# Performance work log

Measured on AMD Instinct MI355X. Metric: run time of the kernel, lower is better.

## Reference

```python
import jax, jax.numpy as jnp
import numpy as np

MODES = 16

def setup_inputs() -> dict:
    key = jax.random.key(0)
    k1, k2 = jax.random.split(key)
    x = jax.random.normal(k1, (16, 32, 256, 256), dtype=jnp.float32)
    weights = jax.random.normal(k2, (32, 32, MODES, MODES, 2), dtype=jnp.float32) * 0.1
    return {"x": x, "weights": weights}

def reference(x, weights):
    # x: [B, Ci, H, W]; weights: [Ci, Co, m, m, 2]
    B, Ci, H, W = x.shape
    m = weights.shape[2]
    Co = weights.shape[1]
    x_ft = jnp.fft.rfft2(x, axes=(-2, -1))  # [B, Ci, H, W//2+1] complex
    w_c = jax.lax.complex(weights[..., 0], weights[..., 1])  # [Ci, Co, m, m]
    low = jnp.einsum('bixy,ioxy->boxy', x_ft[:, :, :m, :m], w_c)  # [B, Co, m, m]
    out_ft = jnp.zeros((B, Co, H, W // 2 + 1), dtype=x_ft.dtype)
    out_ft = out_ft.at[:, :, :m, :m].set(low)
    return jnp.fft.irfft2(out_ft, s=(H, W), axes=(-2, -1)).astype(x.dtype)
```

## Files before the change

### kernel.cpp

```cpp
#include <hip/hip_runtime.h>

typedef float v4 __attribute__((ext_vector_type(4)));
typedef float f32x4 __attribute__((ext_vector_type(4)));
typedef short bf16x8 __attribute__((ext_vector_type(8)));

#define TWO_PI_256 0.024543692606170259f


__device__ __forceinline__ unsigned short f2bf(float f) {
  const unsigned int u = __float_as_uint(f);
  return (unsigned short)((u + 0x7fffu + ((u >> 16) & 1u)) >> 16);
}
__device__ __forceinline__ float bf2f(unsigned short h) {
  return __uint_as_float(((unsigned int)h) << 16);
}

__global__ __launch_bounds__(256) void k0_trig(unsigned short* __restrict__ Th,
                                               unsigned short* __restrict__ Tl,
                                               unsigned short* __restrict__ Bh,
                                               unsigned short* __restrict__ Bl) {
  const int k = threadIdx.x;
  const int o = blockIdx.x;
  {
    const int kx = o >> 1, p = o & 1;
    float sv, cv;
    sincosf((float)((kx * k) & 255) * TWO_PI_256, &sv, &cv);
    const float val = p ? -sv : cv;
    const unsigned short hi = f2bf(val);
    Th[o * 256 + k] = hi;
    Tl[o * 256 + k] = f2bf(val - bf2f(hi));
  }
  {
    const int idx = o * 256 + k;
    const int nt = idx >> 9;
    const int lane = (idx >> 3) & 63;
    const int j = idx & 7;
    const int q = lane >> 4;
    const int n16 = lane & 15;
    const int kk = q * 8 + j;
    const int w = nt * 16 + n16;
    float val;
    if (kk == 0) {
      val = 1.f / 65536.f;
    } else if (kk == 16) {
      val = 0.f;
    } else {
      const int kx = kk & 15;
      float sv, cv;
      sincosf((float)((kx * w) & 255) * TWO_PI_256, &sv, &cv);
      val = (kk < 16 ? 2.f * cv : -2.f * sv) * (1.f / 65536.f);
    }
    const unsigned short hi = f2bf(val);
    Bh[idx] = hi;
    Bl[idx] = f2bf(val - bf2f(hi));
  }
}

typedef __attribute__((address_space(1))) const unsigned int gas_u32;
typedef __attribute__((address_space(3))) unsigned int las_u32;

__global__ __launch_bounds__(256) void k12_dft(const float* __restrict__ x,
                                               const unsigned short* __restrict__ Th,
                                               const unsigned short* __restrict__ Tl,
                                               float* __restrict__ X) {
  __shared__ __align__(16) float SXF[256 * 34];
  __shared__ __align__(16) unsigned short Ts[2][32 * 264];
  const int tid = threadIdx.x;
  const int lane = tid & 63;
  const int w = tid >> 6;
  const long bc = blockIdx.x;
  {
    const int o = tid >> 3, kb = (tid & 7) * 32;
#pragma unroll
    for (int f = 0; f < 2; ++f) {
      const unsigned short* src = (f ? Tl : Th) + o * 256 + kb;
      unsigned short* dst = &Ts[f][o * 264 + kb];
#pragma unroll
      for (int j = 0; j < 32; j += 8)
        *(bf16x8*)(dst + j) = *(const bf16x8*)(src + j);
    }
  }
  const int q = lane >> 4;
  const int n16 = lane & 15;
  const int ucol = (lane & 7) ^ (lane >> 3);
  f32x4 acc[4][2] = {};
  for (int kc = 0; kc < 256; kc += 32) {
    __syncthreads();
#pragma unroll
    for (int i = 0; i < 8; ++i) {
      const int r0 = w * 64 + i * 8;
      __builtin_amdgcn_global_load_lds(
          (gas_u32*)(x + (bc * 256 + r0 + (lane >> 3)) * 256 + kc + ucol * 4),
          (las_u32*)((unsigned int*)SXF + r0 * 32), 16, 0, 0);
    }
    __syncthreads();
    bf16x8 bh[2], bl[2];
#pragma unroll
    for (int nt = 0; nt < 2; ++nt) {
      const int o = nt * 16 + n16;
      bh[nt] = *(const bf16x8*)&Ts[0][o * 264 + kc + q * 8];
      bl[nt] = *(const bf16x8*)&Ts[1][o * 264 + kc + q * 8];
    }
#pragma unroll
    for (int mt = 0; mt < 4; ++mt) {
      const int m = w * 64 + mt * 16 + n16;
      const int s = n16 & 7;
      const v4 a0 = *(const v4*)&SXF[m * 32 + ((2 * q) ^ s) * 4];
      const v4 a1 = *(const v4*)&SXF[m * 32 + ((2 * q + 1) ^ s) * 4];
      const float af[8] = {a0[0], a0[1], a0[2], a0[3], a1[0], a1[1], a1[2], a1[3]};
      bf16x8 ah, al;
#pragma unroll
      for (int j = 0; j < 8; ++j) {
        const unsigned short h = f2bf(af[j]);
        ah[j] = (short)h;
        al[j] = (short)f2bf(af[j] - bf2f(h));
      }
#pragma unroll
      for (int nt = 0; nt < 2; ++nt) {
        acc[mt][nt] = __builtin_amdgcn_mfma_f32_16x16x32_bf16(ah, bh[nt], acc[mt][nt], 0, 0, 0);
        acc[mt][nt] = __builtin_amdgcn_mfma_f32_16x16x32_bf16(al, bh[nt], acc[mt][nt], 0, 0, 0);
        acc[mt][nt] = __builtin_amdgcn_mfma_f32_16x16x32_bf16(ah, bl[nt], acc[mt][nt], 0, 0, 0);
      }
    }
  }
  __syncthreads();
#pragma unroll
  for (int mt = 0; mt < 4; ++mt)
#pragma unroll
    for (int nt = 0; nt < 2; ++nt)
#pragma unroll
      for (int r = 0; r < 4; ++r)
        SXF[(w * 64 + mt * 16 + q * 4 + r) * 34 + nt * 16 + n16] = acc[mt][nt][r];
  __syncthreads();
  {
    const int kx = tid & 15;
    const int ky = tid >> 4;
    float sn, cs;
    sincosf((float)ky * TWO_PI_256, &sn, &cs);
    float wr = 1.f, wi = 0.f;
    float xr = 0.f, xi = 0.f;
#pragma unroll 8
    for (int h = 0; h < 256; ++h) {
      const float2 f = *(const float2*)&SXF[h * 34 + 2 * kx];
      xr += f.x * wr + f.y * wi;
      xi += f.y * wr - f.x * wi;
      const float nwr = wr * cs - wi * sn;
      const float nwi = wr * sn + wi * cs;
      wr = nwr;
      wi = nwi;
    }
    *(float2*)&X[(bc * 256 + tid) * 2] = make_float2(xr, xi);
  }
}

__global__ __launch_bounds__(512) void kB_mixinv(const float* __restrict__ X,
                                                 const float* __restrict__ Wt,
                                                 const unsigned short* __restrict__ Bh,
                                                 const unsigned short* __restrict__ Bl,
                                                 float* __restrict__ out) {
  __shared__ float2 tbl[256];
  __shared__ float2 Yp[2][256];
  __shared__ float Gs[256][36];
  const int tid = threadIdx.x;
  const int lane = tid & 63;
  const int wv = tid >> 6;
  const int co = blockIdx.x;
  const int b = blockIdx.y;
  const long bc = b * 32 + co;
  const int t2 = tid & 255;
  const int hf = tid >> 8;
  if (hf == 0) {
    float sv, cv;
    sincosf((float)t2 * TWO_PI_256, &sv, &cv);
    tbl[t2] = make_float2(cv, sv);
  }
  {
    float yr = 0.f, yi = 0.f;
    const float2* Xp = (const float2*)X + ((long)b * 8192 + t2);
    const float2* Wp = (const float2*)Wt + ((long)co * 256 + t2);
#pragma unroll 8
    for (int ci = hf * 16; ci < hf * 16 + 16; ++ci) {
      const float2 xv = Xp[ci * 256];
      const float2 wv2 = Wp[ci * 8192];
      yr += xv.x * wv2.x - xv.y * wv2.y;
      yi += xv.x * wv2.y + xv.y * wv2.x;
    }
    Yp[hf][t2] = make_float2(yr, yi);
  }
  __syncthreads();
  if (tid < 256) {
    const float2 a = Yp[0][tid], c = Yp[1][tid];
    Yp[0][tid] = make_float2(a.x + c.x, a.y + c.y);
  }
  __syncthreads();
  {
    const int h = tid >> 1;
    const int p = tid & 1;
    float gr[8] = {}, gi[8] = {};
#pragma unroll 4
    for (int ky = 0; ky < 16; ++ky) {
      const float2 wt = tbl[(ky * h) & 255];
#pragma unroll
      for (int i = 0; i < 8; ++i) {
        const float2 yv = Yp[0][ky * 16 + p * 8 + i];
        gr[i] += yv.x * wt.x - yv.y * wt.y;
        gi[i] += yv.x * wt.y + yv.y * wt.x;
      }
    }
#pragma unroll
    for (int i = 0; i < 8; ++i) {
      const int kx = p * 8 + i;
      Gs[h][kx] = gr[i];
      Gs[h][16 + kx] = gi[i];
    }
  }
  __syncthreads();
  const int q = lane >> 4;
  const int n16 = lane & 15;
  bf16x8 ah[2], al[2];
#pragma unroll
  for (int mt = 0; mt < 2; ++mt) {
    const float* ap = &Gs[wv * 32 + mt * 16 + n16][q * 8];
    const v4 a0 = *(const v4*)ap;
    const v4 a1 = *(const v4*)(ap + 4);
    const float af[8] = {a0[0], a0[1], a0[2], a0[3], a1[0], a1[1], a1[2], a1[3]};
#pragma unroll
    for (int j = 0; j < 8; ++j) {
      const unsigned short hh = f2bf(af[j]);
      ah[mt][j] = (short)hh;
      al[mt][j] = (short)f2bf(af[j] - bf2f(hh));
    }
  }
  float* __restrict__ ob = out + bc * 65536;
#pragma unroll
  for (int nt = 0; nt < 16; ++nt) {
    const bf16x8 bhf = *(const bf16x8*)&Bh[(nt * 64 + lane) * 8];
    const bf16x8 blf = *(const bf16x8*)&Bl[(nt * 64 + lane) * 8];
    f32x4 c0 = {}, c1 = {};
    c0 = __builtin_amdgcn_mfma_f32_16x16x32_bf16(ah[0], bhf, c0, 0, 0, 0);
    c0 = __builtin_amdgcn_mfma_f32_16x16x32_bf16(al[0], bhf, c0, 0, 0, 0);
    c0 = __builtin_amdgcn_mfma_f32_16x16x32_bf16(ah[0], blf, c0, 0, 0, 0);
    c1 = __builtin_amdgcn_mfma_f32_16x16x32_bf16(ah[1], bhf, c1, 0, 0, 0);
    c1 = __builtin_amdgcn_mfma_f32_16x16x32_bf16(al[1], bhf, c1, 0, 0, 0);
    c1 = __builtin_amdgcn_mfma_f32_16x16x32_bf16(ah[1], blf, c1, 0, 0, 0);
#pragma unroll
    for (int r = 0; r < 4; ++r) {
      ob[(wv * 32 + q * 4 + r) * 256 + nt * 16 + n16] = c0[r];
      ob[(wv * 32 + 16 + q * 4 + r) * 256 + nt * 16 + n16] = c1[r];
    }
  }
}

extern "C" void kernel_launch(void* const* d_in, const int* in_sizes, int n_in,
                              void* d_out, int out_size, void* d_ws, size_t ws_size,
                              hipStream_t stream) {
  const float* x = (const float*)d_in[0];
  const float* wt = (const float*)d_in[1];
  float* out = (float*)d_out;
  float* X = (float*)d_ws;
  unsigned short* Th = (unsigned short*)(X + 262144);
  unsigned short* Tl = Th + 8192;
  unsigned short* Bh = Tl + 8192;
  unsigned short* Bl = Bh + 8192;
  k0_trig<<<32, 256, 0, stream>>>(Th, Tl, Bh, Bl);
  k12_dft<<<512, 256, 0, stream>>>(x, Th, Tl, X);
  kB_mixinv<<<dim3(32, 16), 512, 0, stream>>>(X, wt, Bh, Bl, out);
}
```

Measured before the change: 265.9 us.

## Fuse twiddle-table generation into DFT kernel and double its threads per block

Removes the separate trig-table kernel. Each DFT block now computes its own bf16 hi/lo cosine/sine table straight into shared memory during the first k-chunk, and the first 32 blocks also write the inverse-basis table used by the later mixing kernel. The block size grows from 256 to 512 threads, so each wave handles half as many rows. This drops one launch and a global round-trip for the tables, at the cost of redundant sincos work in every block and idle threads in the final column-DFT stage.

```diff
diff --git a/kernel.cpp b/kernel.cpp
--- a/kernel.cpp
+++ b/kernel.cpp
@@ -15,83 +15,68 @@
   return __uint_as_float(((unsigned int)h) << 16);
 }
 
-__global__ __launch_bounds__(256) void k0_trig(unsigned short* __restrict__ Th,
-                                               unsigned short* __restrict__ Tl,
+typedef __attribute__((address_space(1))) const unsigned int gas_u32;
+typedef __attribute__((address_space(3))) unsigned int las_u32;
+
+__global__ __launch_bounds__(512) void k12_dft(const float* __restrict__ x,
+                                               float* __restrict__ X,
                                                unsigned short* __restrict__ Bh,
                                                unsigned short* __restrict__ Bl) {
-  const int k = threadIdx.x;
-  const int o = blockIdx.x;
-  {
-    const int kx = o >> 1, p = o & 1;
-    float sv, cv;
-    sincosf((float)((kx * k) & 255) * TWO_PI_256, &sv, &cv);
-    const float val = p ? -sv : cv;
-    const unsigned short hi = f2bf(val);
-    Th[o * 256 + k] = hi;
-    Tl[o * 256 + k] = f2bf(val - bf2f(hi));
-  }
-  {
-    const int idx = o * 256 + k;
-    const int nt = idx >> 9;
-    const int lane = (idx >> 3) & 63;
-    const int j = idx & 7;
-    const int q = lane >> 4;
-    const int n16 = lane & 15;
-    const int kk = q * 8 + j;
-    const int w = nt * 16 + n16;
-    float val;
-    if (kk == 0) {
-      val = 1.f / 65536.f;
-    } else if (kk == 16) {
-      val = 0.f;
-    } else {
-      const int kx = kk & 15;
-      float sv, cv;
-      sincosf((float)((kx * w) & 255) * TWO_PI_256, &sv, &cv);
-      val = (kk < 16 ? 2.f * cv : -2.f * sv) * (1.f / 65536.f);
-    }
-    const unsigned short hi = f2bf(val);
-    Bh[idx] = hi;
-    Bl[idx] = f2bf(val - bf2f(hi));
-  }
-}
-
-typedef __attribute__((address_space(1))) const unsigned int gas_u32;
-typedef __attribute__((address_space(3))) unsigned int las_u32;
-
-__global__ __launch_bounds__(256) void k12_dft(const float* __restrict__ x,
-                                               const unsigned short* __restrict__ Th,
-                                               const unsigned short* __restrict__ Tl,
-                                               float* __restrict__ X) {
   __shared__ __align__(16) float SXF[256 * 34];
   __shared__ __align__(16) unsigned short Ts[2][32 * 264];
   const int tid = threadIdx.x;
   const int lane = tid & 63;
   const int w = tid >> 6;
   const long bc = blockIdx.x;
-  {
-    const int o = tid >> 3, kb = (tid & 7) * 32;
-#pragma unroll
-    for (int f = 0; f < 2; ++f) {
-      const unsigned short* src = (f ? Tl : Th) + o * 256 + kb;
-      unsigned short* dst = &Ts[f][o * 264 + kb];
-#pragma unroll
-      for (int j = 0; j < 32; j += 8)
-        *(bf16x8*)(dst + j) = *(const bf16x8*)(src + j);
-    }
-  }
   const int q = lane >> 4;
   const int n16 = lane & 15;
   const int ucol = (lane & 7) ^ (lane >> 3);
-  f32x4 acc[4][2] = {};
+  f32x4 acc[2][2] = {};
   for (int kc = 0; kc < 256; kc += 32) {
-    __syncthreads();
-#pragma unroll
-    for (int i = 0; i < 8; ++i) {
-      const int r0 = w * 64 + i * 8;
+    if (kc) __syncthreads();
+#pragma unroll
+    for (int i = 0; i < 4; ++i) {
+      const int r0 = w * 32 + i * 8;
       __builtin_amdgcn_global_load_lds(
           (gas_u32*)(x + (bc * 256 + r0 + (lane >> 3)) * 256 + kc + ucol * 4),
           (las_u32*)((unsigned int*)SXF + r0 * 32), 16, 0, 0);
+    }
+    if (kc == 0) {
+      const int o = tid >> 4;
+      const int kxo = o >> 1, p = o & 1;
+      const int kb = (tid & 15) * 16;
+#pragma unroll 4
+      for (int j = 0; j < 16; ++j) {
+        const int k = kb + j;
+        float sv, cv;
+        sincosf((float)((kxo * k) & 255) * TWO_PI_256, &sv, &cv);
+        const float val = p ? -sv : cv;
+        const unsigned short hi = f2bf(val);
+        Ts[0][o * 264 + k] = hi;
+        Ts[1][o * 264 + k] = f2bf(val - bf2f(hi));
+      }
+      if (bc < 32 && tid < 256) {
+        const int idx = (int)bc * 256 + tid;
+        const int nt = idx >> 9;
+        const int bl_ = (idx >> 3) & 63;
+        const int jj = idx & 7;
+        const int kk = (bl_ >> 4) * 8 + jj;
+        const int ww = nt * 16 + (bl_ & 15);
+        float val;
+        if (kk == 0) {
+          val = 1.f / 65536.f;
+        } else if (kk == 16) {
+          val = 0.f;
+        } else {
+          const int kx = kk & 15;
+          float sv, cv;
+          sincosf((float)((kx * ww) & 255) * TWO_PI_256, &sv, &cv);
+          val = (kk < 16 ? 2.f * cv : -2.f * sv) * (1.f / 65536.f);
+        }
+        const unsigned short hi = f2bf(val);
+        Bh[idx] = hi;
+        Bl[idx] = f2bf(val - bf2f(hi));
+      }
     }
     __syncthreads();
     bf16x8 bh[2], bl[2];
@@ -102,8 +87,8 @@
       bl[nt] = *(const bf16x8*)&Ts[1][o * 264 + kc + q * 8];
     }
 #pragma unroll
-    for (int mt = 0; mt < 4; ++mt) {
-      const int m = w * 64 + mt * 16 + n16;
+    for (int mt = 0; mt < 2; ++mt) {
+      const int m = w * 32 + mt * 16 + n16;
       const int s = n16 & 7;
       const v4 a0 = *(const v4*)&SXF[m * 32 + ((2 * q) ^ s) * 4];
       const v4 a1 = *(const v4*)&SXF[m * 32 + ((2 * q + 1) ^ s) * 4];
@@ -125,14 +110,14 @@
   }
   __syncthreads();
 #pragma unroll
-  for (int mt = 0; mt < 4; ++mt)
+  for (int mt = 0; mt < 2; ++mt)
 #pragma unroll
     for (int nt = 0; nt < 2; ++nt)
 #pragma unroll
       for (int r = 0; r < 4; ++r)
-        SXF[(w * 64 + mt * 16 + q * 4 + r) * 34 + nt * 16 + n16] = acc[mt][nt][r];
-  __syncthreads();
-  {
+        SXF[(w * 32 + mt * 16 + q * 4 + r) * 34 + nt * 16 + n16] = acc[mt][nt][r];
+  __syncthreads();
+  if (tid < 256) {
     const int kx = tid & 15;
     const int ky = tid >> 4;
     float sn, cs;
@@ -258,11 +243,8 @@
   const float* wt = (const float*)d_in[1];
   float* out = (float*)d_out;
   float* X = (float*)d_ws;
-  unsigned short* Th = (unsigned short*)(X + 262144);
-  unsigned short* Tl = Th + 8192;
-  unsigned short* Bh = Tl + 8192;
+  unsigned short* Bh = (unsigned short*)(X + 262144);
   unsigned short* Bl = Bh + 8192;
-  k0_trig<<<32, 256, 0, stream>>>(Th, Tl, Bh, Bl);
-  k12_dft<<<512, 256, 0, stream>>>(x, Th, Tl, X);
+  k12_dft<<<512, 512, 0, stream>>>(x, X, Bh, Bl);
   kB_mixinv<<<dim3(32, 16), 512, 0, stream>>>(X, wt, Bh, Bl, out);
 }
```

Result: no change. 264.5 us (-0.5%).
